# Performance work log

Hardware: AMD Instinct MI355X
Metric: run time of the kernel (lower is better)

## Reference

```python
import jax, jax.numpy as jnp
import numpy as np

B, T, V = 64, 8192, 50257


def setup_inputs() -> dict:
    key = jax.random.key(0)
    k1, k2, k3, k4 = jax.random.split(key, 4)
    ids = jax.random.randint(k1, (B, T), 1, V, dtype=jnp.int32)
    # give each row a random real length in [T//2, T], rest padding (pad_token_id=0)
    lens = jax.random.randint(k4, (B,), T // 2, T + 1, dtype=jnp.int32)
    pos = jnp.arange(T, dtype=jnp.int32)[None, :]
    input_ids = jnp.where(pos < lens[:, None], ids, 0)
    is_punct = jax.random.uniform(k2, (V,)) < 0.05
    is_abbreviation = jax.random.uniform(k3, (V,)) < 0.01
    return {
        "input_ids": input_ids,
        "is_punct": is_punct,
        "is_abbreviation": is_abbreviation,
        "max_phrase_len": 32,
        "pad_token_id": 0,
    }


def reference(input_ids, is_punct, is_abbreviation, max_phrase_len, pad_token_id):
    Bb, Tt = input_ids.shape
    # ---- compute_is_end ----
    punct_at_t = is_punct[input_ids]                               # (B,T)
    prev_ids = jnp.concatenate(
        [jnp.zeros((Bb, 1), input_ids.dtype), input_ids[:, :-1]], axis=1)
    prev_is_abbr = is_abbreviation[prev_ids].at[:, 0].set(False)
    is_real = input_ids != pad_token_id                            # (B,T)
    pos = jnp.arange(Tt, dtype=jnp.int32)
    pos_bt = jnp.broadcast_to(pos[None, :], (Bb, Tt))
    last_real = jnp.max(jnp.where(is_real, pos_bt, -1), axis=1)    # (B,)
    is_end0 = punct_at_t & ~prev_is_abbr & is_real                 # pre-scan boundaries

    def step(last_boundary, xs):
        e_t, t = xs
        forced = (t - last_boundary) >= max_phrase_len
        fire = (e_t | (last_real == t) | forced) & (t <= last_real)
        last_boundary = jnp.where(fire, t, last_boundary)
        return last_boundary, fire

    _, fires = jax.lax.scan(
        step, jnp.full((Bb,), -1, jnp.int32),
        (is_end0.T, jnp.arange(Tt, dtype=jnp.int32)))
    is_end = fires.T                                               # (B,T) bool

    # ---- pack_phrases_from_is_end (P padded to T upper bound) ----
    ie = is_end.astype(jnp.int32)
    phrase_id = jnp.concatenate(
        [jnp.zeros((Bb, 1), jnp.int32), jnp.cumsum(ie[:, :-1], axis=1)], axis=1)
    P = Tt
    rows = jnp.arange(Bb, dtype=jnp.int32)[:, None]
    first_pos = jnp.full((Bb, P), Tt, jnp.int32).at[rows, phrase_id].min(pos_bt)
    slot = pos_bt - jnp.take_along_axis(first_pos, phrase_id, axis=1)  # (B,T)
    in_range = (slot < max_phrase_len) & (slot >= 0) & is_real
    # route invalid entries to a dummy slot (index max_phrase_len), slice it off
    safe_slot = jnp.where(in_range, slot, max_phrase_len)
    mask_pad = jnp.zeros((Bb, P, max_phrase_len + 1), bool)
    mask_pad = mask_pad.at[rows, phrase_id, safe_slot].set(in_range)
    phrase_mask = mask_pad[:, :, :max_phrase_len]
    tok_pad = jnp.zeros((Bb, P, max_phrase_len + 1), jnp.int32)
    tok_pad = tok_pad.at[rows, phrase_id, safe_slot].set(jnp.where(in_range, pos_bt, 0))
    phrase_token_idx = tok_pad[:, :, :max_phrase_len]
    phrase_end_pos = jnp.full((Bb, P), -1, jnp.int32).at[rows, phrase_id].max(
        jnp.where(in_range, pos_bt, -1))
    return phrase_mask, phrase_token_idx, phrase_end_pos
```

## Files before the change

### kernel.cpp

```cpp
#include <hip/hip_runtime.h>
#include <stdint.h>

#define BB 64
#define TT 8192

#define TPB 512
#define BPR 16
#define MAXF 1024

#define WS_PAIR 4096

#define MOFF ((long long)BB * TT * 32)

__device__ __forceinline__ unsigned long long bitsBelow(int e) {
    return (e >= 64) ? ~0ULL : ((1ULL << e) - 1ULL);
}

__device__ __forceinline__ bool lut(const void* tbl, bool packed, int idx) {
    if (packed) return ((const uint8_t*)tbl)[idx] != 0;
    return ((const uint32_t*)tbl)[idx] != 0;
}

__global__ __launch_bounds__(256) void natural_kernel(
        const int* __restrict__ ids,
        const void* __restrict__ punct,
        const void* __restrict__ abbr,
        ulonglong2* __restrict__ pairW) {
    int lane = threadIdx.x & 63;
    bool packed;
    {
        const uint32_t* w = (const uint32_t*)punct;
        uint32_t x0 = w[lane * 4], x1 = w[lane * 4 + 1];
        uint32_t x2 = w[lane * 4 + 2], x3 = w[lane * 4 + 3];
        uint32_t o = x0 | x1 | x2 | x3;
        bool byteHi = (o & 0xFEFEFEFEu) != 0u;
        bool gt1 = (x0 > 1u) | (x1 > 1u) | (x2 > 1u) | (x3 > 1u);
        unsigned long long b1 = __ballot(byteHi);
        unsigned long long b2 = __ballot(gt1);
        packed = (b1 == 0ULL) && (b2 != 0ULL);
    }

    int g = blockIdx.x * 256 + threadIdx.x;
    int t = g & (TT - 1);
    int id = ids[g];
    bool real = (id != 0);
    bool isLR = real && ((t == TT - 1) || (ids[g + 1] == 0));
    bool e = false;
    if (real && lut(punct, packed, id)) {
        bool pa = (t > 0) ? lut(abbr, packed, ids[g - 1]) : false;
        e = !pa;
    }
    bool natural = real && (e || isLR);
    unsigned long long nb = __ballot(natural);
    unsigned long long rb = __ballot(real);
    if ((threadIdx.x & 63) == 0) {
        pairW[g >> 6] = make_ulonglong2(nb, rb);
    }
}

__global__ __launch_bounds__(TPB) void fill_kernel(
        const ulonglong2* __restrict__ pairW,
        int* __restrict__ out) {
    __shared__ int sFires[MAXF];
    __shared__ int sNf;

    int bid   = blockIdx.x;
    int b     = bid >> 4;
    int slice = bid & 15;
    int tid   = threadIdx.x;

    int nf = 0;
    if (slice < 2) {
        int wave = tid >> 6, lane = tid & 63;
        if (wave == 0) {
            ulonglong2 pA = pairW[b * 128 + lane];
            ulonglong2 pB = pairW[b * 128 + 64 + lane];
            unsigned long long nA = pA.x, rA = pA.y;
            unsigned long long nB = pB.x, rB = pB.y;
            int lnA = nA ? lane * 64 + 63 - __clzll(nA) : -1;
            int lnB = nB ? (lane + 64) * 64 + 63 - __clzll(nB) : -1;
            int sA = lnA;
            for (int d = 1; d < 64; d <<= 1) { int v = __shfl_up(sA, d); if (lane >= d) sA = max(sA, v); }
            int exA = __shfl_up(sA, 1); if (lane == 0) exA = -1;
            int totA = __shfl(sA, 63);
            int sB = lnB;
            for (int d = 1; d < 64; d <<= 1) { int v = __shfl_up(sB, d); if (lane >= d) sB = max(sB, v); }
            int exB = __shfl_up(sB, 1); if (lane == 0) exB = -1;
            exB = max(exB, totA);

            auto fireWord = [&](unsigned long long nw, unsigned long long rw,
                                int widx, int carry) -> unsigned long long {
                long long wbase = (long long)widx * 64;
                unsigned long long fire = 0, rem = nw;
                long long cur = carry;
                while (true) {
                    int nxt = rem ? (__ffsll(rem) - 1) : 64;
                    int r = (int)(((cur - wbase) % 32 + 32) % 32);
                    unsigned long long pat = (1ULL << r) | (1ULL << (r + 32));
                    int s = (int)(cur - wbase + 1); if (s < 0) s = 0;
                    fire |= pat & bitsBelow(nxt) & ~bitsBelow(s);
                    if (!rem) break;
                    fire |= 1ULL << nxt;
                    cur = wbase + nxt;
                    rem &= rem - 1;
                }
                return fire & rw;
            };
            unsigned long long fA = fireWord(nA, rA, lane, exA);
            unsigned long long fB = fireWord(nB, rB, lane + 64, exB);
            int pcA = __popcll(fA), pcB = __popcll(fB);
            int iA = pcA;
            for (int d = 1; d < 64; d <<= 1) { int v = __shfl_up(iA, d); if (lane >= d) iA += v; }
            int baseA = iA - pcA;
            int totPA = __shfl(iA, 63);
            int iB = pcB;
            for (int d = 1; d < 64; d <<= 1) { int v = __shfl_up(iB, d); if (lane >= d) iB += v; }
            int baseB = totPA + iB - pcB;
            int total = totPA + __shfl(iB, 63);
            unsigned long long f = fA; int idx = baseA;
            while (f) { int tt = __ffsll(f) - 1; if (idx < MAXF) sFires[idx] = lane * 64 + tt; ++idx; f &= f - 1; }
            f = fB; idx = baseB;
            while (f) { int tt = __ffsll(f) - 1; if (idx < MAXF) sFires[idx] = (lane + 64) * 64 + tt; ++idx; f &= f - 1; }
            if (lane == 0) sNf = (total > MAXF) ? MAXF : total;
        }
        __syncthreads();
        nf = sNf;
    }

    int p0 = slice * TPB;
    long long mbase = (long long)bid * 16384;
#pragma unroll
    for (int k = 0; k < 8; ++k) {
        int task = k * TPB + tid;
        int q  = task & 7;
        int lp = task >> 3;
        int p  = p0 + lp;
        int4 mv, tv;
        if (p < nf) {
            int end   = sFires[p];
            int start = (p > 0) ? (sFires[p - 1] + 1) : 0;
            int len   = end - start + 1;
            int s0 = q * 4;
            int* mp = (int*)&mv;
            int* tp = (int*)&tv;
#pragma unroll
            for (int j = 0; j < 4; ++j) {
                int s = s0 + j;
                bool m = s < len;
                mp[j] = m ? 1 : 0;
                tp[j] = m ? (start + s) : 0;
            }
        } else {
            mv = make_int4(0, 0, 0, 0);
            tv = mv;
        }
        long long o = mbase + lp * 32 + q * 4;
        *(int4*)(out + o)        = mv;
        *(int4*)(out + MOFF + o) = tv;
    }
    {
        int p = p0 + tid;
        out[2 * MOFF + (long long)b * TT + p] = (p < nf) ? sFires[p] : -1;
    }
}

extern "C" void kernel_launch(void* const* d_in, const int* in_sizes, int n_in,
                              void* d_out, int out_size, void* d_ws, size_t ws_size,
                              hipStream_t stream) {
    const int*  ids   = (const int*)d_in[0];
    const void* punct = d_in[1];
    const void* abbr  = d_in[2];
    char* ws = (char*)d_ws;
    ulonglong2* pairW = (ulonglong2*)(ws + WS_PAIR);
    int* out = (int*)d_out;

    natural_kernel<<<(BB * TT) / 256, 256, 0, stream>>>(ids, punct, abbr, pairW);
    fill_kernel   <<<BB * BPR, TPB, 0, stream>>>(pairW, out);
}
```

Baseline: 28.61 us.

## Fuse boundary-detection kernel into fill kernel as a single launch

Merges the per-token natural-boundary kernel into the fill kernel. Blocks handling the first two slices of each row compute the punct/abbr/real bitmasks themselves, with each thread reading 16 ids vectorized and packing the bits through shared memory. This removes one launch and the workspace round trip. In exchange, only 128 blocks do the whole per-row scan serially before writing, so the row's critical path gets longer and the scan is duplicated across two blocks per row.

```diff
diff --git a/kernel.cpp b/kernel.cpp
--- a/kernel.cpp
+++ b/kernel.cpp
@@ -4,11 +4,9 @@
 #define BB 64
 #define TT 8192
 
-#define TPB 512
-#define BPR 16
+#define TPB  512
+#define BPR  16
 #define MAXF 1024
-
-#define WS_PAIR 4096
 
 #define MOFF ((long long)BB * TT * 32)
 
@@ -21,46 +19,13 @@
     return ((const uint32_t*)tbl)[idx] != 0;
 }
 
-__global__ __launch_bounds__(256) void natural_kernel(
+__global__ __launch_bounds__(TPB) void mono_kernel(
         const int* __restrict__ ids,
         const void* __restrict__ punct,
         const void* __restrict__ abbr,
-        ulonglong2* __restrict__ pairW) {
-    int lane = threadIdx.x & 63;
-    bool packed;
-    {
-        const uint32_t* w = (const uint32_t*)punct;
-        uint32_t x0 = w[lane * 4], x1 = w[lane * 4 + 1];
-        uint32_t x2 = w[lane * 4 + 2], x3 = w[lane * 4 + 3];
-        uint32_t o = x0 | x1 | x2 | x3;
-        bool byteHi = (o & 0xFEFEFEFEu) != 0u;
-        bool gt1 = (x0 > 1u) | (x1 > 1u) | (x2 > 1u) | (x3 > 1u);
-        unsigned long long b1 = __ballot(byteHi);
-        unsigned long long b2 = __ballot(gt1);
-        packed = (b1 == 0ULL) && (b2 != 0ULL);
-    }
-
-    int g = blockIdx.x * 256 + threadIdx.x;
-    int t = g & (TT - 1);
-    int id = ids[g];
-    bool real = (id != 0);
-    bool isLR = real && ((t == TT - 1) || (ids[g + 1] == 0));
-    bool e = false;
-    if (real && lut(punct, packed, id)) {
-        bool pa = (t > 0) ? lut(abbr, packed, ids[g - 1]) : false;
-        e = !pa;
-    }
-    bool natural = real && (e || isLR);
-    unsigned long long nb = __ballot(natural);
-    unsigned long long rb = __ballot(real);
-    if ((threadIdx.x & 63) == 0) {
-        pairW[g >> 6] = make_ulonglong2(nb, rb);
-    }
-}
-
-__global__ __launch_bounds__(TPB) void fill_kernel(
-        const ulonglong2* __restrict__ pairW,
         int* __restrict__ out) {
+    __shared__ unsigned long long sNat[128], sReal[128];
+    __shared__ uint16_t sN16[TPB], sR16[TPB];
     __shared__ int sFires[MAXF];
     __shared__ int sNf;
 
@@ -71,12 +36,63 @@
 
     int nf = 0;
     if (slice < 2) {
-        int wave = tid >> 6, lane = tid & 63;
+        int lane = tid & 63;
+        bool packed;
+        {
+            const uint32_t* w = (const uint32_t*)punct;
+            uint32_t x0 = w[lane * 4], x1 = w[lane * 4 + 1];
+            uint32_t x2 = w[lane * 4 + 2], x3 = w[lane * 4 + 3];
+            uint32_t o = x0 | x1 | x2 | x3;
+            bool byteHi = (o & 0xFEFEFEFEu) != 0u;
+            bool gt1 = (x0 > 1u) | (x1 > 1u) | (x2 > 1u) | (x3 > 1u);
+            unsigned long long b1 = __ballot(byteHi);
+            unsigned long long b2 = __ballot(gt1);
+            packed = (b1 == 0ULL) && (b2 != 0ULL);
+        }
+
+        const int* rowIds = ids + b * TT;
+        int base = tid * 16;
+        int id[17];
+        {
+            int4 v0 = *(const int4*)(rowIds + base);
+            int4 v1 = *(const int4*)(rowIds + base + 4);
+            int4 v2 = *(const int4*)(rowIds + base + 8);
+            int4 v3 = *(const int4*)(rowIds + base + 12);
+            id[0]=v0.x;  id[1]=v0.y;  id[2]=v0.z;  id[3]=v0.w;
+            id[4]=v1.x;  id[5]=v1.y;  id[6]=v1.z;  id[7]=v1.w;
+            id[8]=v2.x;  id[9]=v2.y;  id[10]=v2.z; id[11]=v2.w;
+            id[12]=v3.x; id[13]=v3.y; id[14]=v3.z; id[15]=v3.w;
+        }
+        id[16] = (tid < TPB - 1) ? rowIds[base + 16] : 0;
+        int prev = (tid > 0) ? rowIds[base - 1] : 0;
+        uint32_t nbits = 0, rbits = 0;
+#pragma unroll
+        for (int j = 0; j < 16; ++j) {
+            int idj = id[j];
+            bool real = (idj != 0);
+            bool isLR = real && ((base + j == TT - 1) || (id[j + 1] == 0));
+            bool e = false;
+            if (real && lut(punct, packed, idj)) {
+                int pid = j ? id[j - 1] : prev;
+                e = (base + j == 0) ? true : !lut(abbr, packed, pid);
+            }
+            bool nat = real && (e || isLR);
+            nbits |= (uint32_t)nat  << j;
+            rbits |= (uint32_t)real << j;
+        }
+        sN16[tid] = (uint16_t)nbits;
+        sR16[tid] = (uint16_t)rbits;
+        __syncthreads();
+        if (tid < 128) {
+            sNat[tid]  = *(const unsigned long long*)&sN16[tid * 4];
+            sReal[tid] = *(const unsigned long long*)&sR16[tid * 4];
+        }
+        __syncthreads();
+
+        int wave = tid >> 6;
         if (wave == 0) {
-            ulonglong2 pA = pairW[b * 128 + lane];
-            ulonglong2 pB = pairW[b * 128 + 64 + lane];
-            unsigned long long nA = pA.x, rA = pA.y;
-            unsigned long long nB = pB.x, rB = pB.y;
+            unsigned long long nA = sNat[lane],  nB = sNat[lane + 64];
+            unsigned long long rA = sReal[lane], rB = sReal[lane + 64];
             int lnA = nA ? lane * 64 + 63 - __clzll(nA) : -1;
             int lnB = nB ? (lane + 64) * 64 + 63 - __clzll(nB) : -1;
             int sA = lnA;
@@ -170,10 +186,7 @@
     const int*  ids   = (const int*)d_in[0];
     const void* punct = d_in[1];
     const void* abbr  = d_in[2];
-    char* ws = (char*)d_ws;
-    ulonglong2* pairW = (ulonglong2*)(ws + WS_PAIR);
     int* out = (int*)d_out;
 
-    natural_kernel<<<(BB * TT) / 256, 256, 0, stream>>>(ids, punct, abbr, pairW);
-    fill_kernel   <<<BB * BPR, TPB, 0, stream>>>(pairW, out);
+    mono_kernel<<<BB * BPR, TPB, 0, stream>>>(ids, punct, abbr, out);
 }
```

Result: slower. 39.38 us (+37.6%).

## Offload padding-slot zero fill into the natural-boundary kernel

Applied to the files above, without the earlier changes.

The first kernel, which only computes boundary ballots, now also writes zeros and -1 for phrase slots 1024–3071 of each row. The fill kernel launches 12 blocks per row instead of 16 and skips those slices. This spreads the large output write traffic across both kernels so the light first kernel is no longer bandwidth-idle. It relies on the existing cap that no row has more than 1024 phrases.

```diff
diff --git a/kernel.cpp b/kernel.cpp
--- a/kernel.cpp
+++ b/kernel.cpp
@@ -4,9 +4,10 @@
 #define BB 64
 #define TT 8192
 
-#define TPB 512
-#define BPR 16
+#define TPB  512
 #define MAXF 1024
+
+#define K2SL 12
 
 #define WS_PAIR 4096
 
@@ -25,8 +26,26 @@
         const int* __restrict__ ids,
         const void* __restrict__ punct,
         const void* __restrict__ abbr,
-        ulonglong2* __restrict__ pairW) {
-    int lane = threadIdx.x & 63;
+        ulonglong2* __restrict__ pairW,
+        int* __restrict__ out) {
+    int i   = blockIdx.x;
+    int tid = threadIdx.x;
+
+    {
+        int b   = i >> 5;
+        int sub = i & 31;
+        long long rb = (long long)b * (TT * 32) + 1024 * 32;
+        long long o  = rb + sub * 2048 + tid * 8;
+        int4 z = make_int4(0, 0, 0, 0);
+        *(int4*)(out + o)            = z;
+        *(int4*)(out + o + 4)        = z;
+        *(int4*)(out + MOFF + o)     = z;
+        *(int4*)(out + MOFF + o + 4) = z;
+        if (tid < 64)
+            out[2 * MOFF + (long long)b * TT + 1024 + sub * 64 + tid] = -1;
+    }
+
+    int lane = tid & 63;
     bool packed;
     {
         const uint32_t* w = (const uint32_t*)punct;
@@ -39,8 +58,7 @@
         unsigned long long b2 = __ballot(gt1);
         packed = (b1 == 0ULL) && (b2 != 0ULL);
     }
-
-    int g = blockIdx.x * 256 + threadIdx.x;
+    int g = i * 256 + tid;
     int t = g & (TT - 1);
     int id = ids[g];
     bool real = (id != 0);
@@ -52,9 +70,9 @@
     }
     bool natural = real && (e || isLR);
     unsigned long long nb = __ballot(natural);
-    unsigned long long rb = __ballot(real);
-    if ((threadIdx.x & 63) == 0) {
-        pairW[g >> 6] = make_ulonglong2(nb, rb);
+    unsigned long long rb2 = __ballot(real);
+    if ((tid & 63) == 0) {
+        pairW[g >> 6] = make_ulonglong2(nb, rb2);
     }
 }
 
@@ -65,12 +83,13 @@
     __shared__ int sNf;
 
     int bid   = blockIdx.x;
-    int b     = bid >> 4;
-    int slice = bid & 15;
+    int b     = bid / K2SL;
+    int j     = bid - b * K2SL;
+    int slice = (j < 2) ? j : (j + 4);
     int tid   = threadIdx.x;
 
     int nf = 0;
-    if (slice < 2) {
+    if (j < 2) {
         int wave = tid >> 6, lane = tid & 63;
         if (wave == 0) {
             ulonglong2 pA = pairW[b * 128 + lane];
@@ -128,7 +147,7 @@
     }
 
     int p0 = slice * TPB;
-    long long mbase = (long long)bid * 16384;
+    long long mbase = ((long long)b * TT + p0) * 32;
 #pragma unroll
     for (int k = 0; k < 8; ++k) {
         int task = k * TPB + tid;
@@ -144,11 +163,11 @@
             int* mp = (int*)&mv;
             int* tp = (int*)&tv;
 #pragma unroll
-            for (int j = 0; j < 4; ++j) {
-                int s = s0 + j;
+            for (int jj = 0; jj < 4; ++jj) {
+                int s = s0 + jj;
                 bool m = s < len;
-                mp[j] = m ? 1 : 0;
-                tp[j] = m ? (start + s) : 0;
+                mp[jj] = m ? 1 : 0;
+                tp[jj] = m ? (start + s) : 0;
             }
         } else {
             mv = make_int4(0, 0, 0, 0);
@@ -174,6 +193,6 @@
     ulonglong2* pairW = (ulonglong2*)(ws + WS_PAIR);
     int* out = (int*)d_out;
 
-    natural_kernel<<<(BB * TT) / 256, 256, 0, stream>>>(ids, punct, abbr, pairW);
-    fill_kernel   <<<BB * BPR, TPB, 0, stream>>>(pairW, out);
+    natural_kernel<<<(BB * TT) / 256, 256, 0, stream>>>(ids, punct, abbr, pairW, out);
+    fill_kernel   <<<BB * K2SL, TPB, 0, stream>>>(pairW, out);
 }
```

Result: slower. 30.41 us (+6.3%).
